# Kernel optimization log

Hardware: AMD Instinct MI355X
Metric: run time of the kernel (lower is better)

Reference implementation:

```python
import jax, jax.numpy as jnp
import numpy as np

B, N, C = 64, 320, 768
H = 12
D = C // H  # 64 head dim


def setup_inputs() -> dict:
    key = jax.random.key(0)
    k1, k2, k3, k4, k5 = jax.random.split(key, 5)
    s = 0.02
    return {
        "x": jax.random.normal(k1, (B, N, C), jnp.float32),
        "w_qkv": jax.random.normal(k2, (3 * C, C), jnp.float32) * s,
        "b_qkv": jax.random.normal(k3, (3 * C,), jnp.float32) * s,
        "w_proj": jax.random.normal(k4, (C, C), jnp.float32) * s,
        "b_proj": jax.random.normal(k5, (C,), jnp.float32) * s,
        "num_t": 64,
        "num_s": 256,
    }


def reference(x, w_qkv, b_qkv, w_proj, b_proj, num_t, num_s):
    Bx, Nx, Cx = x.shape
    scale = 1.0 / jnp.sqrt(jnp.asarray(D, x.dtype))
    # qkv projection: [B,N,3C] -> [3,B,H,N,D]
    qkv = x @ w_qkv.T + b_qkv
    qkv = qkv.reshape(Bx, Nx, 3, H, D).transpose(2, 0, 3, 1, 4)
    q, k, v = qkv[0], qkv[1], qkv[2]
    q_t, q_s = q[:, :, :num_t], q[:, :, num_t:]
    k_t = k[:, :, :num_t]
    v_t = v[:, :, :num_t]
    # template self-attention: [B,H,num_t,num_t]
    attn_t = jax.nn.softmax(jnp.einsum("bhqd,bhkd->bhqk", q_t, k_t) * scale, axis=-1)
    x_t = jnp.einsum("bhqk,bhkd->bhqd", attn_t, v_t)
    x_t = x_t.transpose(0, 2, 1, 3).reshape(Bx, num_t, Cx)
    # search attends to all tokens: [B,H,num_s,N]
    attn_s = jax.nn.softmax(jnp.einsum("bhqd,bhkd->bhqk", q_s, k) * scale, axis=-1)
    x_s = jnp.einsum("bhqk,bhkd->bhqd", attn_s, v)
    x_s = x_s.transpose(0, 2, 1, 3).reshape(Bx, num_s, Cx)
    out = jnp.concatenate([x_t, x_s], axis=1)
    return out @ w_proj.T + b_proj
```

## Files before the change

kernel.cpp:

```cpp
#include <hip/hip_runtime.h>
#include <hip/hip_bf16.h>


typedef __attribute__((ext_vector_type(8))) short short8;
typedef __attribute__((ext_vector_type(4))) float f32x4;
typedef __hip_bfloat16 bf16;

#define NTOK 320
#define CDIM 768
#define NHEAD 12
#define MFMA16(a,b,c) __builtin_amdgcn_mfma_f32_16x16x32_bf16((a),(b),(c),0,0,0)

__device__ __forceinline__ unsigned short bfbits(float v) {
    bf16 h = __float2bfloat16(v);
    unsigned short u; __builtin_memcpy(&u, &h, 2);
    return u;
}

__device__ __forceinline__ short8 ldfrag(const bf16* p) { return *(const short8*)p; }
__device__ __forceinline__ short8 ldfrag(const float* p) {
    float4 a = *(const float4*)p;
    float4 b = *(const float4*)(p + 4);
    short8 r;
    r[0]=(short)bfbits(a.x); r[1]=(short)bfbits(a.y); r[2]=(short)bfbits(a.z); r[3]=(short)bfbits(a.w);
    r[4]=(short)bfbits(b.x); r[5]=(short)bfbits(b.y); r[6]=(short)bfbits(b.z); r[7]=(short)bfbits(b.w);
    return r;
}

__device__ __forceinline__ void stage16(const bf16* g, bf16* l) {
    __builtin_amdgcn_global_load_lds(
        (const __attribute__((address_space(1))) void*)g,
        (__attribute__((address_space(3))) void*)l, 16, 0, 0);
}

__global__ __launch_bounds__(256) void cvt3_kernel(const float* __restrict__ s0, bf16* __restrict__ d0, int n0,
                                                   const float* __restrict__ s1, bf16* __restrict__ d1, int n1,
                                                   const float* __restrict__ s2, bf16* __restrict__ d2, int n2)
{
    const int ntot = n0 + n1 + n2;
    int i = blockIdx.x * 256 + threadIdx.x;
    const int stride = gridDim.x * 256;
    for (; i < ntot; i += stride) {
        const float* s; bf16* d; int j = i;
        if (j < n0)              { s = s0; d = d0; }
        else if ((j -= n0) < n1) { s = s1; d = d1; }
        else                     { j -= n1; s = s2; d = d2; }
        const float4 a = ((const float4*)s)[2 * (size_t)j];
        const float4 b = ((const float4*)s)[2 * (size_t)j + 1];
        short8 r;
        r[0]=(short)bfbits(a.x); r[1]=(short)bfbits(a.y); r[2]=(short)bfbits(a.z); r[3]=(short)bfbits(a.w);
        r[4]=(short)bfbits(b.x); r[5]=(short)bfbits(b.y); r[6]=(short)bfbits(b.z); r[7]=(short)bfbits(b.w);
        ((short8*)d)[j] = r;
    }
}

template<int NOUT, int EPI, int BF16B>
__global__ __launch_bounds__(256) void gemm_bt16(const bf16* __restrict__ A,
                                                 const void* __restrict__ Bmv,
                                                 const float* __restrict__ bias,
                                                 void* __restrict__ o0,
                                                 void* __restrict__ o1,
                                                 void* __restrict__ o2)
{
    __shared__ alignas(16) bf16 As[128 * 32];
    __shared__ alignas(16) bf16 Bs[128 * 32];
    const int tid  = threadIdx.x;
    const int lane = tid & 63;
    const int wv   = tid >> 6;
    const int r16  = lane & 15;
    const int kg   = lane >> 4;

    constexpr int GX  = NOUT / 128;
    constexpr int NWG = GX * 160;
    int flat = blockIdx.y * GX + blockIdx.x;
    flat = (flat & 7) * (NWG >> 3) + (flat >> 3);
    const int byy = flat / GX;
    const int bxx = flat - byy * GX;
    const int m0  = byy * 128;
    const int n0  = bxx * 128;
    const int wm  = (wv & 1) * 64;
    const int wn  = (wv >> 1) * 64;

    const bf16*  Ab   = A + (size_t)m0 * CDIM;
    const bf16*  Bb16 = (const bf16*)Bmv  + (size_t)n0 * CDIM;
    const float* Bb32 = (const float*)Bmv + (size_t)n0 * CDIM;

    const int ra0 = tid >> 2;
    const int ca0 = (tid & 3) * 8;

    bf16* lA0 = &As[(size_t)(wv * 64) * 8];
    bf16* lA1 = &As[(size_t)(wv * 64 + 256) * 8];
    bf16* lB0 = &Bs[(size_t)(wv * 64) * 8];
    bf16* lB1 = &Bs[(size_t)(wv * 64 + 256) * 8];

    f32x4 acc[4][4] = {};

    for (int k0 = 0; k0 < CDIM; k0 += 32) {
        if constexpr (BF16B) {
            __syncthreads();
            stage16(Ab   + (size_t)ra0        * CDIM + k0 + ca0, lA0);
            stage16(Ab   + (size_t)(ra0 + 64) * CDIM + k0 + ca0, lA1);
            stage16(Bb16 + (size_t)ra0        * CDIM + k0 + ca0, lB0);
            stage16(Bb16 + (size_t)(ra0 + 64) * CDIM + k0 + ca0, lB1);
            __syncthreads();
        } else {
            short8 gb0 = ldfrag(Bb32 + (size_t)ra0        * CDIM + k0 + ca0);
            short8 gb1 = ldfrag(Bb32 + (size_t)(ra0 + 64) * CDIM + k0 + ca0);
            __syncthreads();
            stage16(Ab + (size_t)ra0        * CDIM + k0 + ca0, lA0);
            stage16(Ab + (size_t)(ra0 + 64) * CDIM + k0 + ca0, lA1);
            *(short8*)&Bs[(size_t)tid * 8]         = gb0;
            *(short8*)&Bs[(size_t)(tid + 256) * 8] = gb1;
            __syncthreads();
        }

        short8 af[4], bfr[4];
        #pragma unroll
        for (int mt = 0; mt < 4; mt++)
            af[mt] = *(const short8*)&As[(wm + mt * 16 + r16) * 32 + kg * 8];
        #pragma unroll
        for (int nt = 0; nt < 4; nt++)
            bfr[nt] = *(const short8*)&Bs[(wn + nt * 16 + r16) * 32 + kg * 8];
        #pragma unroll
        for (int mt = 0; mt < 4; mt++)
            #pragma unroll
            for (int nt = 0; nt < 4; nt++)
                acc[mt][nt] = MFMA16(af[mt], bfr[nt], acc[mt][nt]);
    }

    #pragma unroll
    for (int nt = 0; nt < 4; nt++) {
        const int gn = n0 + wn + nt * 16 + r16;
        const float bv = bias[gn];
        if (EPI == 0) {
            const int which = gn / CDIM;
            const int rem   = gn - which * CDIM;
            const int hh    = rem >> 6;
            const int dd    = rem & 63;
            #pragma unroll
            for (int mt = 0; mt < 4; mt++) {
                const int gm0  = m0 + wm + mt * 16 + kg * 4;
                const int bidx = gm0 / NTOK;
                const int nn0  = gm0 - bidx * NTOK;
                float v[4];
                #pragma unroll
                for (int r = 0; r < 4; r++) v[r] = acc[mt][nt][r] + bv;
                if (which == 0) {
                    bf16* q = (bf16*)o0 + ((size_t)(bidx * NHEAD + hh) * NTOK + nn0) * 64 + dd;
                    #pragma unroll
                    for (int r = 0; r < 4; r++) q[(size_t)r * 64] = __float2bfloat16(v[r]);
                } else if (which == 1) {
                    bf16* k = (bf16*)o1 + ((size_t)(bidx * NHEAD + hh) * NTOK + nn0) * 64 + dd;
                    #pragma unroll
                    for (int r = 0; r < 4; r++) k[(size_t)r * 64] = __float2bfloat16(v[r]);
                } else {
                    ushort4 p;
                    unsigned short* ps = (unsigned short*)&p;
                    #pragma unroll
                    for (int r = 0; r < 4; r++) ps[r] = bfbits(v[r]);
                    *(ushort4*)((bf16*)o2 + ((size_t)(bidx * NHEAD + hh) * 64 + dd) * NTOK + nn0) = p;
                }
            }
        } else {
            float* out = (float*)o0;
            #pragma unroll
            for (int mt = 0; mt < 4; mt++) {
                const int gm0 = m0 + wm + mt * 16 + kg * 4;
                #pragma unroll
                for (int r = 0; r < 4; r++)
                    out[(size_t)(gm0 + r) * NOUT + gn] = acc[mt][nt][r] + bv;
            }
        }
    }
}

#define SW 324
#define ATTN_NWG (768 * 10)
__global__ __launch_bounds__(256) void attn_kernel(const bf16* __restrict__ q_ws,
                                                   const bf16* __restrict__ k_ws,
                                                   const bf16* __restrict__ vt_ws,
                                                   bf16* __restrict__ attn,
                                                   const int* __restrict__ numt_p)
{
    __shared__ alignas(16) float S[32 * SW];
    __shared__ float rowstat[32];
    int num_t = 64;
    if (numt_p) {
        int v = *numt_p;
        float f = __int_as_float(v);
        if (v >= 1 && v <= 319) num_t = v;
        else if (f >= 1.f && f <= 319.f) num_t = (int)f;
    }
    if (num_t <= 0 || num_t > NTOK || (num_t & 31)) num_t = 64;

    const int tid  = threadIdx.x;
    const int lane = tid & 63;
    const int w    = tid >> 6;
    const int r16  = lane & 15;
    const int kg   = lane >> 4;

    int blk = blockIdx.x;
    blk = (blk & 7) * (ATTN_NWG / 8) + (blk >> 3);
    const int bh  = blk / 10;
    const int qt  = blk - bh * 10;
    const int b   = bh / NHEAD;
    const int h   = bh - b * NHEAD;
    const int q0  = qt * 32;
    const int nk  = (q0 + 32 <= num_t) ? num_t : NTOK;
    const int nk16 = nk >> 4;

    const bf16* qp = q_ws  + (size_t)bh * NTOK * 64;
    const bf16* kp = k_ws  + (size_t)bh * NTOK * 64;
    const bf16* vp = vt_ws + (size_t)bh * 64 * NTOK;

    short8 qf[2][2];
    #pragma unroll
    for (int ks = 0; ks < 2; ks++)
        #pragma unroll
        for (int mt = 0; mt < 2; mt++)
            qf[ks][mt] = ldfrag(qp + (size_t)(q0 + mt * 16 + r16) * 64 + ks * 32 + kg * 8);

    const float scale = 0.125f;
    for (int nt = w; nt < nk16; nt += 4) {
        f32x4 a0 = {}, a1 = {};
        #pragma unroll
        for (int ks = 0; ks < 2; ks++) {
            short8 kf = ldfrag(kp + (size_t)(nt * 16 + r16) * 64 + ks * 32 + kg * 8);
            a0 = MFMA16(qf[ks][0], kf, a0);
            a1 = MFMA16(qf[ks][1], kf, a1);
        }
        #pragma unroll
        for (int r = 0; r < 4; r++) {
            S[(kg * 4 + r) * SW + nt * 16 + r16]      = a0[r] * scale;
            S[(16 + kg * 4 + r) * SW + nt * 16 + r16] = a1[r] * scale;
        }
    }
    __syncthreads();

    {
        const int row = tid >> 3;
        const int sub = tid & 7;
        float* Sr = S + row * SW;
        bf16*  Pr = (bf16*)Sr;
        float mx = -1e30f;
        for (int c = sub * 4; c < nk; c += 32) {
            float4 t = *(float4*)&Sr[c];
            mx = fmaxf(mx, fmaxf(fmaxf(t.x, t.y), fmaxf(t.z, t.w)));
        }
        #pragma unroll
        for (int m = 1; m < 8; m <<= 1) mx = fmaxf(mx, __shfl_xor(mx, m));
        float sum = 0.f;
        for (int c = sub * 4; c < nk; c += 32) {
            float4 t = *(float4*)&Sr[c];
            t.x = __expf(t.x - mx); t.y = __expf(t.y - mx);
            t.z = __expf(t.z - mx); t.w = __expf(t.w - mx);
            sum += t.x + t.y + t.z + t.w;
            ushort4 p;
            p.x = bfbits(t.x); p.y = bfbits(t.y); p.z = bfbits(t.z); p.w = bfbits(t.w);
            *(ushort4*)&Pr[c] = p;
        }
        #pragma unroll
        for (int m = 1; m < 8; m <<= 1) sum += __shfl_xor(sum, m);
        if (sub == 0) rowstat[row] = 1.0f / sum;
    }
    __syncthreads();

    const int mt  = w & 1;
    const int ntb = w >> 1;
    const bf16* Pb = (const bf16*)S;
    f32x4 o[2] = {};
    for (int ks = 0; ks < (nk >> 5); ks++) {
        short8 af = *(const short8*)&Pb[(size_t)(mt * 16 + r16) * (SW * 2) + ks * 32 + kg * 8];
        #pragma unroll
        for (int i = 0; i < 2; i++) {
            const int nt = ntb + i * 2;
            short8 vf = ldfrag(vp + (size_t)(nt * 16 + r16) * NTOK + ks * 32 + kg * 8);
            o[i] = MFMA16(af, vf, o[i]);
        }
    }
    #pragma unroll
    for (int i = 0; i < 2; i++) {
        const int nt = ntb + i * 2;
        const int dd = nt * 16 + r16;
        #pragma unroll
        for (int r = 0; r < 4; r++) {
            const int qrow  = mt * 16 + kg * 4 + r;
            const float val = o[i][r] * rowstat[qrow];
            const int token = q0 + qrow;
            attn[(((size_t)b * NTOK + token) * NHEAD + h) * 64 + dd] = __float2bfloat16(val);
        }
    }
}

extern "C" void kernel_launch(void* const* d_in, const int* in_sizes, int n_in,
                              void* d_out, int out_size, void* d_ws, size_t ws_size,
                              hipStream_t stream)
{
    float* out = (float*)d_out;

    const float *x = nullptr, *w_qkv = nullptr, *b_qkv = nullptr,
                *w_proj = nullptr, *b_proj = nullptr;
    const int* numt_p = nullptr;
    for (int i = 0; i < n_in; i++) {
        switch (in_sizes[i]) {
            case 15728640: x      = (const float*)d_in[i]; break;
            case 1769472:  w_qkv  = (const float*)d_in[i]; break;
            case 2304:     b_qkv  = (const float*)d_in[i]; break;
            case 589824:   w_proj = (const float*)d_in[i]; break;
            case 768:      b_proj = (const float*)d_in[i]; break;
            case 1:        if (!numt_p) numt_p = (const int*)d_in[i]; break;
            default: break;
        }
    }
    if (!x || !w_qkv || !b_qkv || !w_proj || !b_proj) return;

    const size_t per      = (size_t)64 * NHEAD * NTOK * 64;
    const size_t wq_elems = (size_t)2304 * 768;
    const size_t wp_elems = (size_t)768 * 768;
    const size_t base_need = 4 * per * sizeof(bf16);
    const size_t full_need = base_need + (wq_elems + wp_elems) * sizeof(bf16);
    if (ws_size < base_need) return;
    const bool full = ws_size >= full_need;

    bf16* q_ws  = (bf16*)d_ws;
    bf16* k_ws  = q_ws  + per;
    bf16* vt_ws = k_ws  + per;
    bf16* attn  = vt_ws + per;
    bf16* x16   = attn;
    bf16* wq16  = attn + per;
    bf16* wp16  = wq16 + wq_elems;

    if (full)
        cvt3_kernel<<<2048, 256, 0, stream>>>(x, x16, (int)(per / 8),
                                              w_qkv, wq16, (int)(wq_elems / 8),
                                              w_proj, wp16, (int)(wp_elems / 8));
    else
        cvt3_kernel<<<2048, 256, 0, stream>>>(x, x16, (int)(per / 8),
                                              x, x16, 0, x, x16, 0);

    if (full)
        gemm_bt16<2304, 0, 1><<<dim3(18, 160), 256, 0, stream>>>(
            x16, wq16, b_qkv, q_ws, k_ws, vt_ws);
    else
        gemm_bt16<2304, 0, 0><<<dim3(18, 160), 256, 0, stream>>>(
            x16, w_qkv, b_qkv, q_ws, k_ws, vt_ws);

    attn_kernel<<<ATTN_NWG, 256, 0, stream>>>(q_ws, k_ws, vt_ws, attn, numt_p);

    if (full)
        gemm_bt16<768, 1, 1><<<dim3(6, 160), 256, 0, stream>>>(
            attn, wp16, b_proj, out, nullptr, nullptr);
    else
        gemm_bt16<768, 1, 0><<<dim3(6, 160), 256, 0, stream>>>(
            attn, w_proj, b_proj, out, nullptr, nullptr);
}
```

Baseline: 389.8 us.

## Swizzle attention LDS tile, drop padding to fit four blocks per CU

Replaces the padded 324-wide score buffer with an unpadded 320-wide buffer that uses an XOR swizzle to avoid bank conflicts. The separate rowstat array goes away: each row's reciprocal sum is stored in an unused slot of that row. This shrinks LDS per block so four 256-thread blocks can be resident, matching the new launch_bounds(256,4) hint. The full-length QK and PV loops are also fully unrolled. The cost is more complex index arithmetic, a tighter register budget, and reliance on the spare-slot placement staying clear of the bf16 probability data.

```diff
diff --git a/kernel.cpp b/kernel.cpp
--- a/kernel.cpp
+++ b/kernel.cpp
@@ -174,16 +174,14 @@
     }
 }
 
-#define SW 324
 #define ATTN_NWG (768 * 10)
-__global__ __launch_bounds__(256) void attn_kernel(const bf16* __restrict__ q_ws,
-                                                   const bf16* __restrict__ k_ws,
-                                                   const bf16* __restrict__ vt_ws,
-                                                   bf16* __restrict__ attn,
-                                                   const int* __restrict__ numt_p)
+__global__ __launch_bounds__(256, 4) void attn_kernel(const bf16* __restrict__ q_ws,
+                                                      const bf16* __restrict__ k_ws,
+                                                      const bf16* __restrict__ vt_ws,
+                                                      bf16* __restrict__ attn,
+                                                      const int* __restrict__ numt_p)
 {
-    __shared__ alignas(16) float S[32 * SW];
-    __shared__ float rowstat[32];
+    __shared__ alignas(16) float S[32 * 320];
     int num_t = 64;
     if (numt_p) {
         int v = *numt_p;
@@ -221,7 +219,7 @@
             qf[ks][mt] = ldfrag(qp + (size_t)(q0 + mt * 16 + r16) * 64 + ks * 32 + kg * 8);
 
     const float scale = 0.125f;
-    for (int nt = w; nt < nk16; nt += 4) {
+    auto p1body = [&](int nt) {
         f32x4 a0 = {}, a1 = {};
         #pragma unroll
         for (int ks = 0; ks < 2; ks++) {
@@ -229,54 +227,73 @@
             a0 = MFMA16(qf[ks][0], kf, a0);
             a1 = MFMA16(qf[ks][1], kf, a1);
         }
+        const int col = nt * 16 + r16;
         #pragma unroll
         for (int r = 0; r < 4; r++) {
-            S[(kg * 4 + r) * SW + nt * 16 + r16]      = a0[r] * scale;
-            S[(16 + kg * 4 + r) * SW + nt * 16 + r16] = a1[r] * scale;
-        }
+            const int ro  = kg * 4 + r;
+            const int swz = (ro & 7) << 2;
+            S[ro * 320        + (col ^ swz)] = a0[r] * scale;
+            S[(16 + ro) * 320 + (col ^ swz)] = a1[r] * scale;
+        }
+    };
+    if (nk16 == 20) {
+        #pragma unroll
+        for (int it = 0; it < 5; it++) p1body(w + it * 4);
+    } else {
+        for (int nt = w; nt < nk16; nt += 4) p1body(nt);
     }
     __syncthreads();
 
     {
         const int row = tid >> 3;
         const int sub = tid & 7;
-        float* Sr = S + row * SW;
+        const int swzw = (row & 7) << 2;
+        const int swzh = (row & 7) << 3;
+        float* Sr = S + row * 320;
         bf16*  Pr = (bf16*)Sr;
         float mx = -1e30f;
         for (int c = sub * 4; c < nk; c += 32) {
-            float4 t = *(float4*)&Sr[c];
+            float4 t = *(float4*)&Sr[c ^ swzw];
             mx = fmaxf(mx, fmaxf(fmaxf(t.x, t.y), fmaxf(t.z, t.w)));
         }
         #pragma unroll
         for (int m = 1; m < 8; m <<= 1) mx = fmaxf(mx, __shfl_xor(mx, m));
         float sum = 0.f;
         for (int c = sub * 4; c < nk; c += 32) {
-            float4 t = *(float4*)&Sr[c];
+            float4 t = *(float4*)&Sr[c ^ swzw];
             t.x = __expf(t.x - mx); t.y = __expf(t.y - mx);
             t.z = __expf(t.z - mx); t.w = __expf(t.w - mx);
             sum += t.x + t.y + t.z + t.w;
             ushort4 p;
             p.x = bfbits(t.x); p.y = bfbits(t.y); p.z = bfbits(t.z); p.w = bfbits(t.w);
-            *(ushort4*)&Pr[c] = p;
+            *(ushort4*)&Pr[c ^ swzh] = p;
         }
         #pragma unroll
         for (int m = 1; m < 8; m <<= 1) sum += __shfl_xor(sum, m);
-        if (sub == 0) rowstat[row] = 1.0f / sum;
+        if (sub == 0) Sr[316 ^ swzw] = 1.0f / sum;
     }
     __syncthreads();
 
     const int mt  = w & 1;
     const int ntb = w >> 1;
-    const bf16* Pb = (const bf16*)S;
+    const int prow = mt * 16 + r16;
+    const bf16* Pbr = (const bf16*)(S + prow * 320);
+    const int pswzh = (prow & 7) << 3;
     f32x4 o[2] = {};
-    for (int ks = 0; ks < (nk >> 5); ks++) {
-        short8 af = *(const short8*)&Pb[(size_t)(mt * 16 + r16) * (SW * 2) + ks * 32 + kg * 8];
+    auto p3body = [&](int ks) {
+        short8 af = *(const short8*)&Pbr[(ks * 32 + kg * 8) ^ pswzh];
         #pragma unroll
         for (int i = 0; i < 2; i++) {
             const int nt = ntb + i * 2;
             short8 vf = ldfrag(vp + (size_t)(nt * 16 + r16) * NTOK + ks * 32 + kg * 8);
             o[i] = MFMA16(af, vf, o[i]);
         }
+    };
+    if (nk == NTOK) {
+        #pragma unroll
+        for (int ks = 0; ks < 10; ks++) p3body(ks);
+    } else {
+        for (int ks = 0; ks < (nk >> 5); ks++) p3body(ks);
     }
     #pragma unroll
     for (int i = 0; i < 2; i++) {
@@ -285,7 +302,8 @@
         #pragma unroll
         for (int r = 0; r < 4; r++) {
             const int qrow  = mt * 16 + kg * 4 + r;
-            const float val = o[i][r] * rowstat[qrow];
+            const float invs = S[qrow * 320 + (316 ^ ((qrow & 7) << 2))];
+            const float val = o[i][r] * invs;
             const int token = q0 + qrow;
             attn[(((size_t)b * NTOK + token) * NHEAD + h) * 64 + dd] = __float2bfloat16(val);
         }
```

New measurement: 382.2 us. About the same (-1.9%).
